# Optimization experiments

Measured on AMD Instinct MI355X. Metric: run time of the kernel, lower is better.

## Reference

```python
import jax, jax.numpy as jnp
import numpy as np

jax.config.update("jax_enable_x64", True)  # original upcasts to double for cdist

B, D, T = 16, 256, 2048
K = 1024  # num_embeddings
COMMITMENT_COST = 0.25


def setup_inputs() -> dict:
    key = jax.random.key(0)
    k1, k2 = jax.random.split(key)
    inputs = jax.random.normal(k1, (B, D, T), dtype=jnp.float32)
    embeddings = jax.random.uniform(k2, (K, D), minval=-1.0 / K, maxval=1.0 / K, dtype=jnp.float32)
    return {"inputs": inputs, "embeddings": embeddings}


def reference(inputs, embeddings):
    b, d, t = inputs.shape
    # [B, D, T] -> [B*T, D]
    flat = jnp.transpose(inputs, (0, 2, 1)).reshape(-1, d)
    # fp64 pairwise squared distances (argmin identical to cdist p=2)
    x = flat.astype(jnp.float64)
    e = embeddings.astype(jnp.float64)
    d2 = (jnp.sum(x * x, axis=1, keepdims=True)
          - 2.0 * (x @ e.T)
          + jnp.sum(e * e, axis=1))  # [N, K]
    encoding_indices = jnp.argmin(d2, axis=1)  # [N]
    quantized = embeddings[encoding_indices].reshape(b, t, d).transpose(0, 2, 1)  # [B, D, T]
    q_detached = jax.lax.stop_gradient(quantized)
    e_latent_loss = jnp.mean((q_detached - inputs) ** 2)
    q_latent_loss = jnp.mean((quantized - jax.lax.stop_gradient(inputs)) ** 2)
    loss = q_latent_loss + COMMITMENT_COST * e_latent_loss
    # straight-through estimator
    quantized_st = inputs + jax.lax.stop_gradient(quantized - inputs)
    return quantized_st, loss, e_latent_loss, q_latent_loss, encoding_indices
```

## Files before the change

kernel.cpp:

```cpp
#include <hip/hip_runtime.h>
#include <hip/hip_bf16.h>

#define NB 16
#define ND 256
#define NT 2048
#define NK 1024
#define NN (NB * NT)
#define QSIZE (NB * ND * NT)
#define SCL_OFF QSIZE
#define IDX_OFF (QSIZE + 3)
#define TAU 4.0e-5f

#define WS_CNT   8
#define WS_E2F   1024
#define WS_E2D   8192
#define WS_IDX   16384
#define WS_LIST  147456
#define WS_BPACK 278528
#define WS_PART  1327104

typedef __attribute__((ext_vector_type(8))) short bf16x8;
typedef __attribute__((ext_vector_type(4))) float f32x4;
#define MFMA16(a, b, c) __builtin_amdgcn_mfma_f32_16x16x32_bf16(a, b, c, 0, 0, 0)

__device__ inline void bf16split(float v, short& hi, short& lo) {
    union { __hip_bfloat16 b; short s; } uh, ul;
    uh.b = __float2bfloat16(v);
    float hf = __bfloat162float(uh.b);
    ul.b = __float2bfloat16(v - hf);
    hi = uh.s; lo = ul.s;
}

__global__ __launch_bounds__(64) void vq_e2(const float4* __restrict__ E4,
                                            double* __restrict__ e2d,
                                            float* __restrict__ e2f,
                                            int* __restrict__ cnt) {
    int k = blockIdx.x;
    int lane = threadIdx.x;
    float4 v = E4[k * 64 + lane];
    double s = (double)v.x * v.x + (double)v.y * v.y + (double)v.z * v.z + (double)v.w * v.w;
    #pragma unroll
    for (int off = 32; off; off >>= 1) s += __shfl_down(s, off, 64);
    if (lane == 0) { e2d[k] = s; e2f[k] = (float)s; }
    if (k == 0 && lane == 0) cnt[0] = 0;
}

__global__ __launch_bounds__(64) void vq_prep_bpack(const float4* __restrict__ E4,
                                                    uint4* __restrict__ Bp4) {
    const int cc = blockIdx.x >> 3;
    const int ds = blockIdx.x & 7;
    const int lane = threadIdx.x;
    const int c = cc * 16 + (lane & 15);
    const int q = lane >> 4;
    float4 v0 = E4[(size_t)c * 64 + ds * 8 + q * 2];
    float4 v1 = E4[(size_t)c * 64 + ds * 8 + q * 2 + 1];
    float vals[8] = {v0.x, v0.y, v0.z, v0.w, v1.x, v1.y, v1.z, v1.w};
    union { short s[8]; uint4 v; } hi, lo;
    #pragma unroll
    for (int j = 0; j < 8; ++j) bf16split(vals[j], hi.s[j], lo.s[j]);
    Bp4[(size_t)cc * 1024 + ds * 64 + lane]       = hi.v;
    Bp4[(size_t)cc * 1024 + 512 + ds * 64 + lane] = lo.v;
}

__global__ __launch_bounds__(256, 1) void vq_pass1(const float* __restrict__ X,
                                                   const uint4* __restrict__ Bp4,
                                                   const float* __restrict__ e2f,
                                                   int* __restrict__ idx_ws,
                                                   int* __restrict__ cnt,
                                                   int* __restrict__ list,
                                                   float* __restrict__ out) {
    __shared__ uint4 Bl4[2][1024];
    const int tid  = threadIdx.x;
    const int lane = tid & 63;
    const int w    = tid >> 6;
    const int n0   = blockIdx.x * 128;
    const int b    = n0 >> 11;
    const int t0   = n0 & (NT - 1);
    const int m16  = lane & 15;
    const int q    = lane >> 4;

    bf16x8 ah[2][8], al[2][8];
    const float* Xb = X + (size_t)b * (ND * NT);
    #pragma unroll
    for (int t = 0; t < 2; ++t) {
        const int trow = t0 + w * 32 + t * 16 + m16;
        #pragma unroll
        for (int ds = 0; ds < 8; ++ds) {
            #pragma unroll
            for (int j = 0; j < 8; ++j) {
                const int d = ds * 32 + q * 8 + j;
                float v = Xb[(size_t)d * NT + trow];
                short h, l; bf16split(v, h, l);
                ah[t][ds][j] = h; al[t][ds][j] = l;
            }
        }
    }

    float b1[2][4], b2[2][4]; int i1[2][4];
    #pragma unroll
    for (int t = 0; t < 2; ++t)
        #pragma unroll
        for (int r = 0; r < 4; ++r) { b1[t][r] = 3e38f; b2[t][r] = 3e38f; i1[t][r] = 0; }

    uint4 pre[4];
    #pragma unroll
    for (int i = 0; i < 4; ++i) pre[i] = Bp4[tid + 256 * i];
    #pragma unroll
    for (int i = 0; i < 4; ++i) Bl4[0][tid + 256 * i] = pre[i];
    __syncthreads();

    for (int cc = 0; cc < 64; ++cc) {
        const bf16x8* Bf = (const bf16x8*)Bl4[cc & 1];
        if (cc < 63) {
            #pragma unroll
            for (int i = 0; i < 4; ++i) pre[i] = Bp4[(size_t)(cc + 1) * 1024 + tid + 256 * i];
        }
        f32x4 hh0 = {0.f,0.f,0.f,0.f}, lh0 = {0.f,0.f,0.f,0.f}, hl0 = {0.f,0.f,0.f,0.f};
        f32x4 hh1 = {0.f,0.f,0.f,0.f}, lh1 = {0.f,0.f,0.f,0.f}, hl1 = {0.f,0.f,0.f,0.f};
        #pragma unroll
        for (int ds = 0; ds < 8; ++ds) {
            bf16x8 bh = Bf[ds * 64 + lane];
            bf16x8 bl = Bf[512 + ds * 64 + lane];
            hh0 = MFMA16(ah[0][ds], bh, hh0);
            hh1 = MFMA16(ah[1][ds], bh, hh1);
            lh0 = MFMA16(al[0][ds], bh, lh0);
            lh1 = MFMA16(al[1][ds], bh, lh1);
            hl0 = MFMA16(ah[0][ds], bl, hl0);
            hl1 = MFMA16(ah[1][ds], bl, hl1);
        }
        if (cc < 63) {
            #pragma unroll
            for (int i = 0; i < 4; ++i) Bl4[(cc + 1) & 1][tid + 256 * i] = pre[i];
            __syncthreads();
        }
        const float e2v = e2f[cc * 16 + m16];
        const int  code = cc * 16 + m16;
        #pragma unroll
        for (int r = 0; r < 4; ++r) {
            float s0 = e2v - 2.0f * (hh0[r] + lh0[r] + hl0[r]);
            if (s0 < b1[0][r]) { b2[0][r] = b1[0][r]; b1[0][r] = s0; i1[0][r] = code; }
            else if (s0 < b2[0][r]) b2[0][r] = s0;
            float s1 = e2v - 2.0f * (hh1[r] + lh1[r] + hl1[r]);
            if (s1 < b1[1][r]) { b2[1][r] = b1[1][r]; b1[1][r] = s1; i1[1][r] = code; }
            else if (s1 < b2[1][r]) b2[1][r] = s1;
        }
    }

    #pragma unroll
    for (int t = 0; t < 2; ++t) {
        #pragma unroll
        for (int r = 0; r < 4; ++r) {
            float B1 = b1[t][r], B2 = b2[t][r]; int I1 = i1[t][r];
            #pragma unroll
            for (int mm = 1; mm < 16; mm <<= 1) {
                float o1 = __shfl_xor(B1, mm, 16);
                float o2 = __shfl_xor(B2, mm, 16);
                int   oi = __shfl_xor(I1, mm, 16);
                if (o1 < B1 || (o1 == B1 && oi < I1)) { B2 = fminf(B1, o2); B1 = o1; I1 = oi; }
                else B2 = fminf(B2, o1);
            }
            if (m16 == 0) {
                int n = n0 + w * 32 + t * 16 + q * 4 + r;
                idx_ws[n] = I1;
                out[IDX_OFF + n] = (float)I1;
                if (B2 - B1 < TAU) { int p = atomicAdd(cnt, 1); list[p] = n; }
            }
        }
    }
}

__global__ __launch_bounds__(256, 2) void vq_refine(const float* __restrict__ X,
                                                    const float4* __restrict__ E4,
                                                    const double* __restrict__ e2d,
                                                    const int* __restrict__ cnt,
                                                    const int* __restrict__ list,
                                                    int* __restrict__ idx_ws,
                                                    float* __restrict__ out) {
    __shared__ double xs[4][256];
    __shared__ double sm_s[4][4];
    __shared__ int    sm_k[4][4];
    const int m = cnt[0];
    const int tid = threadIdx.x;
    for (int p = blockIdx.x; p * 4 < m; p += 512) {
        int nrow[4];
        #pragma unroll
        for (int g = 0; g < 4; ++g) {
            int j = p * 4 + g;
            nrow[g] = list[j < m ? j : m - 1];
        }
        #pragma unroll
        for (int g = 0; g < 4; ++g) {
            int n = nrow[g]; int bb = n >> 11; int tt = n & (NT - 1);
            xs[g][tid] = (double)X[((size_t)bb * ND + tid) * NT + tt];
        }
        __syncthreads();
        double acc[4][4];
        #pragma unroll
        for (int kk = 0; kk < 4; ++kk)
            #pragma unroll
            for (int g = 0; g < 4; ++g) acc[kk][g] = 0.0;
        for (int dq = 0; dq < 64; ++dq) {
            double xv[4][4];
            #pragma unroll
            for (int g = 0; g < 4; ++g)
                #pragma unroll
                for (int c = 0; c < 4; ++c) xv[g][c] = xs[g][dq * 4 + c];
            #pragma unroll
            for (int kk = 0; kk < 4; ++kk) {
                float4 ev = E4[(size_t)(kk * 256 + tid) * 64 + dq];
                double e0 = ev.x, e1 = ev.y, e2 = ev.z, e3 = ev.w;
                #pragma unroll
                for (int g = 0; g < 4; ++g)
                    acc[kk][g] += xv[g][0] * e0 + xv[g][1] * e1 + xv[g][2] * e2 + xv[g][3] * e3;
            }
        }
        #pragma unroll
        for (int g = 0; g < 4; ++g) {
            double bs = 1e300; int bk = 0x7fffffff;
            #pragma unroll
            for (int kk = 0; kk < 4; ++kk) {
                int k = kk * 256 + tid;
                double s = e2d[k] - 2.0 * acc[kk][g];
                if (s < bs) { bs = s; bk = k; }
            }
            #pragma unroll
            for (int mm = 1; mm < 64; mm <<= 1) {
                double os = __shfl_xor(bs, mm, 64);
                int    ok = __shfl_xor(bk, mm, 64);
                if (os < bs || (os == bs && ok < bk)) { bs = os; bk = ok; }
            }
            if ((tid & 63) == 0) { sm_s[tid >> 6][g] = bs; sm_k[tid >> 6][g] = bk; }
        }
        __syncthreads();
        if (tid < 4) {
            double Bv = 1e300; int Kv = 0x7fffffff;
            for (int ww = 0; ww < 4; ++ww) {
                double s2 = sm_s[ww][tid]; int k2 = sm_k[ww][tid];
                if (s2 < Bv || (s2 == Bv && k2 < Kv)) { Bv = s2; Kv = k2; }
            }
            if (p * 4 + tid < m) {
                int n = nrow[tid];
                idx_ws[n] = Kv;
                out[IDX_OFF + n] = (float)Kv;
            }
        }
        __syncthreads();
    }
}

__global__ __launch_bounds__(256) void vq_gather(const float* __restrict__ X,
                                                 const float4* __restrict__ E4,
                                                 const int* __restrict__ idx_ws,
                                                 float* __restrict__ out,
                                                 double* __restrict__ part) {
    __shared__ float Eq[32 * 257];
    __shared__ double sm[4];
    const int bt = blockIdx.x;
    const int b  = bt >> 6;
    const int t0 = (bt & 63) << 5;
    const int* irow = idx_ws + b * NT + t0;
    {
        const int r  = threadIdx.x >> 3;
        const int l8 = threadIdx.x & 7;
        const int id = irow[r];
        const float4* er = E4 + (size_t)id * 64;
        #pragma unroll
        for (int it = 0; it < 8; ++it) {
            int c = l8 + (it << 3);
            float4 v = er[c];
            float* p = &Eq[r * 257 + 4 * c];
            p[0] = v.x; p[1] = v.y; p[2] = v.z; p[3] = v.w;
        }
    }
    __syncthreads();
    const int tw = threadIdx.x & 31;
    const int dg = threadIdx.x >> 5;
    double ls = 0.0;
    #pragma unroll 8
    for (int it = 0; it < 32; ++it) {
        const int d = dg + (it << 3);
        const float qv = Eq[tw * 257 + d];
        const size_t off = ((size_t)b * ND + d) * NT + t0 + tw;
        const float x = X[off];
        out[off] = x + (qv - x);
        const double df = (double)qv - (double)x;
        ls = fma(df, df, ls);
    }
    #pragma unroll
    for (int o = 32; o; o >>= 1) ls += __shfl_down(ls, o, 64);
    if ((threadIdx.x & 63) == 0) sm[threadIdx.x >> 6] = ls;
    __syncthreads();
    if (threadIdx.x == 0) part[bt] = sm[0] + sm[1] + sm[2] + sm[3];
}

__global__ __launch_bounds__(256) void vq_final(const double* __restrict__ part,
                                                float* __restrict__ out) {
    __shared__ double sm[4];
    const int tid = threadIdx.x;
    double s = part[tid] + part[tid + 256] + part[tid + 512] + part[tid + 768];
    #pragma unroll
    for (int o = 32; o; o >>= 1) s += __shfl_down(s, o, 64);
    if ((tid & 63) == 0) sm[tid >> 6] = s;
    __syncthreads();
    if (tid == 0) {
        double mse = (sm[0] + sm[1] + sm[2] + sm[3]) * (1.0 / (double)QSIZE);
        out[SCL_OFF + 0] = (float)(1.25 * mse);
        out[SCL_OFF + 1] = (float)mse;
        out[SCL_OFF + 2] = (float)mse;
    }
}

extern "C" void kernel_launch(void* const* d_in, const int* in_sizes, int n_in,
                              void* d_out, int out_size, void* d_ws, size_t ws_size,
                              hipStream_t stream) {
    const float* X = (const float*)d_in[0];
    const float* E = (const float*)d_in[1];
    float* out = (float*)d_out;

    char* ws = (char*)d_ws;
    int*    cnt   = (int*)   (ws + WS_CNT);
    float*  e2f   = (float*) (ws + WS_E2F);
    double* e2d   = (double*)(ws + WS_E2D);
    int*    idxws = (int*)   (ws + WS_IDX);
    int*    list  = (int*)   (ws + WS_LIST);
    uint4*  bpack = (uint4*) (ws + WS_BPACK);
    double* part  = (double*)(ws + WS_PART);

    vq_e2        <<<NK, 64, 0, stream>>>((const float4*)E, e2d, e2f, cnt);
    vq_prep_bpack<<<512, 64, 0, stream>>>((const float4*)E, bpack);
    vq_pass1     <<<NN / 128, 256, 0, stream>>>(X, bpack, e2f, idxws, cnt, list, out);
    vq_refine    <<<512, 256, 0, stream>>>(X, (const float4*)E, e2d, cnt, list, idxws, out);
    vq_gather    <<<NB * (NT / 32), 256, 0, stream>>>(X, (const float4*)E, idxws, out, part);
    vq_final     <<<1, 256, 0, stream>>>(part, out);
}
```

Baseline: 235.8 us.

## Halve pass1 rows per block and transpose codebook for coalesced refine loads

The first-pass MFMA kernel now handles 64 rows per block instead of 128, halving its per-thread register tile and raising launch bounds to two blocks per CU. The grid doubles, so each block reloads the full packed codebook, doubling codebook traffic into shared memory. Separately, the e2 kernel writes a transposed fp32 codebook so the fp64 refine kernel reads contiguous per-thread codes along d, replacing the strided float4 loads. The transpose adds scattered writes in a small prep kernel.

```diff
diff --git a/kernel.cpp b/kernel.cpp
--- a/kernel.cpp
+++ b/kernel.cpp
@@ -17,7 +17,8 @@
 #define WS_IDX   16384
 #define WS_LIST  147456
 #define WS_BPACK 278528
-#define WS_PART  1327104
+#define WS_ET    1327104
+#define WS_PART  2375680
 
 typedef __attribute__((ext_vector_type(8))) short bf16x8;
 typedef __attribute__((ext_vector_type(4))) float f32x4;
@@ -34,10 +35,15 @@
 __global__ __launch_bounds__(64) void vq_e2(const float4* __restrict__ E4,
                                             double* __restrict__ e2d,
                                             float* __restrict__ e2f,
+                                            float* __restrict__ ET,
                                             int* __restrict__ cnt) {
     int k = blockIdx.x;
     int lane = threadIdx.x;
     float4 v = E4[k * 64 + lane];
+    ET[(size_t)(4 * lane + 0) * NK + k] = v.x;
+    ET[(size_t)(4 * lane + 1) * NK + k] = v.y;
+    ET[(size_t)(4 * lane + 2) * NK + k] = v.z;
+    ET[(size_t)(4 * lane + 3) * NK + k] = v.w;
     double s = (double)v.x * v.x + (double)v.y * v.y + (double)v.z * v.z + (double)v.w * v.w;
     #pragma unroll
     for (int off = 32; off; off >>= 1) s += __shfl_down(s, off, 64);
@@ -62,7 +68,7 @@
     Bp4[(size_t)cc * 1024 + 512 + ds * 64 + lane] = lo.v;
 }
 
-__global__ __launch_bounds__(256, 1) void vq_pass1(const float* __restrict__ X,
+__global__ __launch_bounds__(256, 2) void vq_pass1(const float* __restrict__ X,
                                                    const uint4* __restrict__ Bp4,
                                                    const float* __restrict__ e2f,
                                                    int* __restrict__ idx_ws,
@@ -73,17 +79,16 @@
     const int tid  = threadIdx.x;
     const int lane = tid & 63;
     const int w    = tid >> 6;
-    const int n0   = blockIdx.x * 128;
+    const int n0   = blockIdx.x * 64;
     const int b    = n0 >> 11;
     const int t0   = n0 & (NT - 1);
     const int m16  = lane & 15;
     const int q    = lane >> 4;
 
-    bf16x8 ah[2][8], al[2][8];
+    bf16x8 ah[8], al[8];
     const float* Xb = X + (size_t)b * (ND * NT);
-    #pragma unroll
-    for (int t = 0; t < 2; ++t) {
-        const int trow = t0 + w * 32 + t * 16 + m16;
+    {
+        const int trow = t0 + w * 16 + m16;
         #pragma unroll
         for (int ds = 0; ds < 8; ++ds) {
             #pragma unroll
@@ -91,16 +96,14 @@
                 const int d = ds * 32 + q * 8 + j;
                 float v = Xb[(size_t)d * NT + trow];
                 short h, l; bf16split(v, h, l);
-                ah[t][ds][j] = h; al[t][ds][j] = l;
-            }
-        }
-    }
-
-    float b1[2][4], b2[2][4]; int i1[2][4];
-    #pragma unroll
-    for (int t = 0; t < 2; ++t)
-        #pragma unroll
-        for (int r = 0; r < 4; ++r) { b1[t][r] = 3e38f; b2[t][r] = 3e38f; i1[t][r] = 0; }
+                ah[ds][j] = h; al[ds][j] = l;
+            }
+        }
+    }
+
+    float b1[4], b2[4]; int i1[4];
+    #pragma unroll
+    for (int r = 0; r < 4; ++r) { b1[r] = 3e38f; b2[r] = 3e38f; i1[r] = 0; }
 
     uint4 pre[4];
     #pragma unroll
@@ -115,18 +118,14 @@
             #pragma unroll
             for (int i = 0; i < 4; ++i) pre[i] = Bp4[(size_t)(cc + 1) * 1024 + tid + 256 * i];
         }
-        f32x4 hh0 = {0.f,0.f,0.f,0.f}, lh0 = {0.f,0.f,0.f,0.f}, hl0 = {0.f,0.f,0.f,0.f};
-        f32x4 hh1 = {0.f,0.f,0.f,0.f}, lh1 = {0.f,0.f,0.f,0.f}, hl1 = {0.f,0.f,0.f,0.f};
+        f32x4 hh = {0.f,0.f,0.f,0.f}, lh = {0.f,0.f,0.f,0.f}, hl = {0.f,0.f,0.f,0.f};
         #pragma unroll
         for (int ds = 0; ds < 8; ++ds) {
             bf16x8 bh = Bf[ds * 64 + lane];
             bf16x8 bl = Bf[512 + ds * 64 + lane];
-            hh0 = MFMA16(ah[0][ds], bh, hh0);
-            hh1 = MFMA16(ah[1][ds], bh, hh1);
-            lh0 = MFMA16(al[0][ds], bh, lh0);
-            lh1 = MFMA16(al[1][ds], bh, lh1);
-            hl0 = MFMA16(ah[0][ds], bl, hl0);
-            hl1 = MFMA16(ah[1][ds], bl, hl1);
+            hh = MFMA16(ah[ds], bh, hh);
+            lh = MFMA16(al[ds], bh, lh);
+            hl = MFMA16(ah[ds], bl, hl);
         }
         if (cc < 63) {
             #pragma unroll
@@ -137,40 +136,34 @@
         const int  code = cc * 16 + m16;
         #pragma unroll
         for (int r = 0; r < 4; ++r) {
-            float s0 = e2v - 2.0f * (hh0[r] + lh0[r] + hl0[r]);
-            if (s0 < b1[0][r]) { b2[0][r] = b1[0][r]; b1[0][r] = s0; i1[0][r] = code; }
-            else if (s0 < b2[0][r]) b2[0][r] = s0;
-            float s1 = e2v - 2.0f * (hh1[r] + lh1[r] + hl1[r]);
-            if (s1 < b1[1][r]) { b2[1][r] = b1[1][r]; b1[1][r] = s1; i1[1][r] = code; }
-            else if (s1 < b2[1][r]) b2[1][r] = s1;
-        }
-    }
-
-    #pragma unroll
-    for (int t = 0; t < 2; ++t) {
-        #pragma unroll
-        for (int r = 0; r < 4; ++r) {
-            float B1 = b1[t][r], B2 = b2[t][r]; int I1 = i1[t][r];
-            #pragma unroll
-            for (int mm = 1; mm < 16; mm <<= 1) {
-                float o1 = __shfl_xor(B1, mm, 16);
-                float o2 = __shfl_xor(B2, mm, 16);
-                int   oi = __shfl_xor(I1, mm, 16);
-                if (o1 < B1 || (o1 == B1 && oi < I1)) { B2 = fminf(B1, o2); B1 = o1; I1 = oi; }
-                else B2 = fminf(B2, o1);
-            }
-            if (m16 == 0) {
-                int n = n0 + w * 32 + t * 16 + q * 4 + r;
-                idx_ws[n] = I1;
-                out[IDX_OFF + n] = (float)I1;
-                if (B2 - B1 < TAU) { int p = atomicAdd(cnt, 1); list[p] = n; }
-            }
+            float s0 = e2v - 2.0f * (hh[r] + lh[r] + hl[r]);
+            if (s0 < b1[r]) { b2[r] = b1[r]; b1[r] = s0; i1[r] = code; }
+            else if (s0 < b2[r]) b2[r] = s0;
+        }
+    }
+
+    #pragma unroll
+    for (int r = 0; r < 4; ++r) {
+        float B1 = b1[r], B2 = b2[r]; int I1 = i1[r];
+        #pragma unroll
+        for (int mm = 1; mm < 16; mm <<= 1) {
+            float o1 = __shfl_xor(B1, mm, 16);
+            float o2 = __shfl_xor(B2, mm, 16);
+            int   oi = __shfl_xor(I1, mm, 16);
+            if (o1 < B1 || (o1 == B1 && oi < I1)) { B2 = fminf(B1, o2); B1 = o1; I1 = oi; }
+            else B2 = fminf(B2, o1);
+        }
+        if (m16 == 0) {
+            int n = n0 + w * 16 + q * 4 + r;
+            idx_ws[n] = I1;
+            out[IDX_OFF + n] = (float)I1;
+            if (B2 - B1 < TAU) { int p = atomicAdd(cnt, 1); list[p] = n; }
         }
     }
 }
 
 __global__ __launch_bounds__(256, 2) void vq_refine(const float* __restrict__ X,
-                                                    const float4* __restrict__ E4,
+                                                    const float* __restrict__ ET,
                                                     const double* __restrict__ e2d,
                                                     const int* __restrict__ cnt,
                                                     const int* __restrict__ list,
@@ -199,19 +192,19 @@
         for (int kk = 0; kk < 4; ++kk)
             #pragma unroll
             for (int g = 0; g < 4; ++g) acc[kk][g] = 0.0;
-        for (int dq = 0; dq < 64; ++dq) {
-            double xv[4][4];
-            #pragma unroll
-            for (int g = 0; g < 4; ++g)
-                #pragma unroll
-                for (int c = 0; c < 4; ++c) xv[g][c] = xs[g][dq * 4 + c];
-            #pragma unroll
-            for (int kk = 0; kk < 4; ++kk) {
-                float4 ev = E4[(size_t)(kk * 256 + tid) * 64 + dq];
-                double e0 = ev.x, e1 = ev.y, e2 = ev.z, e3 = ev.w;
-                #pragma unroll
-                for (int g = 0; g < 4; ++g)
-                    acc[kk][g] += xv[g][0] * e0 + xv[g][1] * e1 + xv[g][2] * e2 + xv[g][3] * e3;
+        #pragma unroll 2
+        for (int dd = 0; dd < 256; ++dd) {
+            float e0 = ET[(size_t)dd * NK +   0 + tid];
+            float e1 = ET[(size_t)dd * NK + 256 + tid];
+            float e2 = ET[(size_t)dd * NK + 512 + tid];
+            float e3 = ET[(size_t)dd * NK + 768 + tid];
+            #pragma unroll
+            for (int g = 0; g < 4; ++g) {
+                double xv = xs[g][dd];
+                acc[0][g] += xv * (double)e0;
+                acc[1][g] += xv * (double)e1;
+                acc[2][g] += xv * (double)e2;
+                acc[3][g] += xv * (double)e3;
             }
         }
         #pragma unroll
@@ -324,12 +317,13 @@
     int*    idxws = (int*)   (ws + WS_IDX);
     int*    list  = (int*)   (ws + WS_LIST);
     uint4*  bpack = (uint4*) (ws + WS_BPACK);
+    float*  et    = (float*) (ws + WS_ET);
     double* part  = (double*)(ws + WS_PART);
 
-    vq_e2        <<<NK, 64, 0, stream>>>((const float4*)E, e2d, e2f, cnt);
+    vq_e2        <<<NK, 64, 0, stream>>>((const float4*)E, e2d, e2f, et, cnt);
     vq_prep_bpack<<<512, 64, 0, stream>>>((const float4*)E, bpack);
-    vq_pass1     <<<NN / 128, 256, 0, stream>>>(X, bpack, e2f, idxws, cnt, list, out);
-    vq_refine    <<<512, 256, 0, stream>>>(X, (const float4*)E, e2d, cnt, list, idxws, out);
+    vq_pass1     <<<NN / 64, 256, 0, stream>>>(X, bpack, e2f, idxws, cnt, list, out);
+    vq_refine    <<<512, 256, 0, stream>>>(X, et, e2d, cnt, list, idxws, out);
     vq_gather    <<<NB * (NT / 32), 256, 0, stream>>>(X, (const float4*)E, idxws, out, part);
     vq_final     <<<1, 256, 0, stream>>>(part, out);
 }
```

Result: slower. 263.3 us (+11.7%).

## Split codebook across two pass1 blocks, add merge kernel, transpose E for refine

Applied to the files above, without the earlier changes.

Pass1 now launches twice as many blocks, each scanning half of the codebook, and writes per-slice best, second-best and index to workspace. A new merge kernel combines the two slices, writes indices and builds the refine list. Refine can read a transposed fp32 codebook written by vq_e2 for coalesced loads, used when the workspace is large enough, and gather reads indices from the float output. The aim is better occupancy and more parallelism in pass1, at the cost of reloading and re-splitting X per slice and running an extra kernel.

```diff
diff --git a/kernel.cpp b/kernel.cpp
--- a/kernel.cpp
+++ b/kernel.cpp
@@ -11,13 +11,17 @@
 #define IDX_OFF (QSIZE + 3)
 #define TAU 4.0e-5f
 
-#define WS_CNT   8
-#define WS_E2F   1024
-#define WS_E2D   8192
-#define WS_IDX   16384
-#define WS_LIST  147456
-#define WS_BPACK 278528
-#define WS_PART  1327104
+#define WS_CNT   0
+#define WS_PART  64
+#define WS_E2F   8448
+#define WS_E2D   12544
+#define WS_LIST  20736
+#define WS_B1S   151808
+#define WS_B2S   413952
+#define WS_I1S   676096
+#define WS_BPACK 938240
+#define WS_ET    1986816
+#define WS_NEED_ET (WS_ET + 1048576)
 
 typedef __attribute__((ext_vector_type(8))) short bf16x8;
 typedef __attribute__((ext_vector_type(4))) float f32x4;
@@ -34,10 +38,17 @@
 __global__ __launch_bounds__(64) void vq_e2(const float4* __restrict__ E4,
                                             double* __restrict__ e2d,
                                             float* __restrict__ e2f,
+                                            float* __restrict__ ET, int use_et,
                                             int* __restrict__ cnt) {
     int k = blockIdx.x;
     int lane = threadIdx.x;
     float4 v = E4[k * 64 + lane];
+    if (use_et) {
+        ET[(size_t)(4 * lane + 0) * NK + k] = v.x;
+        ET[(size_t)(4 * lane + 1) * NK + k] = v.y;
+        ET[(size_t)(4 * lane + 2) * NK + k] = v.z;
+        ET[(size_t)(4 * lane + 3) * NK + k] = v.w;
+    }
     double s = (double)v.x * v.x + (double)v.y * v.y + (double)v.z * v.z + (double)v.w * v.w;
     #pragma unroll
     for (int off = 32; off; off >>= 1) s += __shfl_down(s, off, 64);
@@ -62,22 +73,23 @@
     Bp4[(size_t)cc * 1024 + 512 + ds * 64 + lane] = lo.v;
 }
 
-__global__ __launch_bounds__(256, 1) void vq_pass1(const float* __restrict__ X,
+__global__ __launch_bounds__(256, 2) void vq_pass1(const float* __restrict__ X,
                                                    const uint4* __restrict__ Bp4,
                                                    const float* __restrict__ e2f,
-                                                   int* __restrict__ idx_ws,
-                                                   int* __restrict__ cnt,
-                                                   int* __restrict__ list,
-                                                   float* __restrict__ out) {
+                                                   float* __restrict__ b1s,
+                                                   float* __restrict__ b2s,
+                                                   int* __restrict__ i1s) {
     __shared__ uint4 Bl4[2][1024];
-    const int tid  = threadIdx.x;
-    const int lane = tid & 63;
-    const int w    = tid >> 6;
-    const int n0   = blockIdx.x * 128;
-    const int b    = n0 >> 11;
-    const int t0   = n0 & (NT - 1);
-    const int m16  = lane & 15;
-    const int q    = lane >> 4;
+    const int tid   = threadIdx.x;
+    const int lane  = tid & 63;
+    const int w     = tid >> 6;
+    const int slice = blockIdx.x & 1;
+    const int n0    = (blockIdx.x >> 1) * 128;
+    const int b     = n0 >> 11;
+    const int t0    = n0 & (NT - 1);
+    const int m16   = lane & 15;
+    const int q     = lane >> 4;
+    const uint4* Bps = Bp4 + (size_t)slice * 32768;
 
     bf16x8 ah[2][8], al[2][8];
     const float* Xb = X + (size_t)b * (ND * NT);
@@ -104,16 +116,16 @@
 
     uint4 pre[4];
     #pragma unroll
-    for (int i = 0; i < 4; ++i) pre[i] = Bp4[tid + 256 * i];
+    for (int i = 0; i < 4; ++i) pre[i] = Bps[tid + 256 * i];
     #pragma unroll
     for (int i = 0; i < 4; ++i) Bl4[0][tid + 256 * i] = pre[i];
     __syncthreads();
 
-    for (int cc = 0; cc < 64; ++cc) {
+    for (int cc = 0; cc < 32; ++cc) {
         const bf16x8* Bf = (const bf16x8*)Bl4[cc & 1];
-        if (cc < 63) {
-            #pragma unroll
-            for (int i = 0; i < 4; ++i) pre[i] = Bp4[(size_t)(cc + 1) * 1024 + tid + 256 * i];
+        if (cc < 31) {
+            #pragma unroll
+            for (int i = 0; i < 4; ++i) pre[i] = Bps[(size_t)(cc + 1) * 1024 + tid + 256 * i];
         }
         f32x4 hh0 = {0.f,0.f,0.f,0.f}, lh0 = {0.f,0.f,0.f,0.f}, hl0 = {0.f,0.f,0.f,0.f};
         f32x4 hh1 = {0.f,0.f,0.f,0.f}, lh1 = {0.f,0.f,0.f,0.f}, hl1 = {0.f,0.f,0.f,0.f};
@@ -128,13 +140,13 @@
             hl0 = MFMA16(ah[0][ds], bl, hl0);
             hl1 = MFMA16(ah[1][ds], bl, hl1);
         }
-        if (cc < 63) {
+        if (cc < 31) {
             #pragma unroll
             for (int i = 0; i < 4; ++i) Bl4[(cc + 1) & 1][tid + 256 * i] = pre[i];
             __syncthreads();
         }
-        const float e2v = e2f[cc * 16 + m16];
-        const int  code = cc * 16 + m16;
+        const int  code = slice * 512 + cc * 16 + m16;
+        const float e2v = e2f[code];
         #pragma unroll
         for (int r = 0; r < 4; ++r) {
             float s0 = e2v - 2.0f * (hh0[r] + lh0[r] + hl0[r]);
@@ -161,20 +173,35 @@
             }
             if (m16 == 0) {
                 int n = n0 + w * 32 + t * 16 + q * 4 + r;
-                idx_ws[n] = I1;
-                out[IDX_OFF + n] = (float)I1;
-                if (B2 - B1 < TAU) { int p = atomicAdd(cnt, 1); list[p] = n; }
-            }
-        }
-    }
+                int s = slice * NN + n;
+                b1s[s] = B1; b2s[s] = B2; i1s[s] = I1;
+            }
+        }
+    }
+}
+
+__global__ __launch_bounds__(256) void vq_merge(const float* __restrict__ b1s,
+                                                const float* __restrict__ b2s,
+                                                const int* __restrict__ i1s,
+                                                int* __restrict__ cnt,
+                                                int* __restrict__ list,
+                                                float* __restrict__ out) {
+    const int n = blockIdx.x * 256 + threadIdx.x;
+    float a1 = b1s[n],      a2 = b2s[n];      int ai = i1s[n];
+    float c1 = b1s[NN + n], c2 = b2s[NN + n]; int ci = i1s[NN + n];
+    float B1, B2; int I1;
+    if (c1 < a1) { B1 = c1; I1 = ci; B2 = fminf(a1, c2); }
+    else         { B1 = a1; I1 = ai; B2 = fminf(a2, c1); }
+    out[IDX_OFF + n] = (float)I1;
+    if (B2 - B1 < TAU) { int p = atomicAdd(cnt, 1); list[p] = n; }
 }
 
 __global__ __launch_bounds__(256, 2) void vq_refine(const float* __restrict__ X,
                                                     const float4* __restrict__ E4,
+                                                    const float* __restrict__ ET, int use_et,
                                                     const double* __restrict__ e2d,
                                                     const int* __restrict__ cnt,
                                                     const int* __restrict__ list,
-                                                    int* __restrict__ idx_ws,
                                                     float* __restrict__ out) {
     __shared__ double xs[4][256];
     __shared__ double sm_s[4][4];
@@ -199,19 +226,32 @@
         for (int kk = 0; kk < 4; ++kk)
             #pragma unroll
             for (int g = 0; g < 4; ++g) acc[kk][g] = 0.0;
-        for (int dq = 0; dq < 64; ++dq) {
-            double xv[4][4];
-            #pragma unroll
-            for (int g = 0; g < 4; ++g)
+        if (use_et) {
+            #pragma unroll 2
+            for (int dd = 0; dd < 256; ++dd) {
+                float e0 = ET[(size_t)dd * NK +   0 + tid];
+                float e1 = ET[(size_t)dd * NK + 256 + tid];
+                float e2 = ET[(size_t)dd * NK + 512 + tid];
+                float e3 = ET[(size_t)dd * NK + 768 + tid];
                 #pragma unroll
-                for (int c = 0; c < 4; ++c) xv[g][c] = xs[g][dq * 4 + c];
-            #pragma unroll
-            for (int kk = 0; kk < 4; ++kk) {
-                float4 ev = E4[(size_t)(kk * 256 + tid) * 64 + dq];
-                double e0 = ev.x, e1 = ev.y, e2 = ev.z, e3 = ev.w;
+                for (int g = 0; g < 4; ++g) {
+                    double xv = xs[g][dd];
+                    acc[0][g] += xv * (double)e0;
+                    acc[1][g] += xv * (double)e1;
+                    acc[2][g] += xv * (double)e2;
+                    acc[3][g] += xv * (double)e3;
+                }
+            }
+        } else {
+            for (int dq = 0; dq < 64; ++dq) {
                 #pragma unroll
-                for (int g = 0; g < 4; ++g)
-                    acc[kk][g] += xv[g][0] * e0 + xv[g][1] * e1 + xv[g][2] * e2 + xv[g][3] * e3;
+                for (int kk = 0; kk < 4; ++kk) {
+                    float4 ev = E4[(size_t)(kk * 256 + tid) * 64 + dq];
+                    #pragma unroll
+                    for (int g = 0; g < 4; ++g)
+                        acc[kk][g] += xs[g][dq*4+0] * (double)ev.x + xs[g][dq*4+1] * (double)ev.y
+                                    + xs[g][dq*4+2] * (double)ev.z + xs[g][dq*4+3] * (double)ev.w;
+                }
             }
         }
         #pragma unroll
@@ -238,11 +278,7 @@
                 double s2 = sm_s[ww][tid]; int k2 = sm_k[ww][tid];
                 if (s2 < Bv || (s2 == Bv && k2 < Kv)) { Bv = s2; Kv = k2; }
             }
-            if (p * 4 + tid < m) {
-                int n = nrow[tid];
-                idx_ws[n] = Kv;
-                out[IDX_OFF + n] = (float)Kv;
-            }
+            if (p * 4 + tid < m) out[IDX_OFF + nrow[tid]] = (float)Kv;
         }
         __syncthreads();
     }
@@ -250,7 +286,6 @@
 
 __global__ __launch_bounds__(256) void vq_gather(const float* __restrict__ X,
                                                  const float4* __restrict__ E4,
-                                                 const int* __restrict__ idx_ws,
                                                  float* __restrict__ out,
                                                  double* __restrict__ part) {
     __shared__ float Eq[32 * 257];
@@ -258,11 +293,11 @@
     const int bt = blockIdx.x;
     const int b  = bt >> 6;
     const int t0 = (bt & 63) << 5;
-    const int* irow = idx_ws + b * NT + t0;
+    const float* irowf = out + IDX_OFF + b * NT + t0;
     {
         const int r  = threadIdx.x >> 3;
         const int l8 = threadIdx.x & 7;
-        const int id = irow[r];
+        const int id = (int)irowf[r];
         const float4* er = E4 + (size_t)id * 64;
         #pragma unroll
         for (int it = 0; it < 8; ++it) {
@@ -319,17 +354,22 @@
 
     char* ws = (char*)d_ws;
     int*    cnt   = (int*)   (ws + WS_CNT);
+    double* part  = (double*)(ws + WS_PART);
     float*  e2f   = (float*) (ws + WS_E2F);
     double* e2d   = (double*)(ws + WS_E2D);
-    int*    idxws = (int*)   (ws + WS_IDX);
     int*    list  = (int*)   (ws + WS_LIST);
+    float*  b1s   = (float*) (ws + WS_B1S);
+    float*  b2s   = (float*) (ws + WS_B2S);
+    int*    i1s   = (int*)   (ws + WS_I1S);
     uint4*  bpack = (uint4*) (ws + WS_BPACK);
-    double* part  = (double*)(ws + WS_PART);
-
-    vq_e2        <<<NK, 64, 0, stream>>>((const float4*)E, e2d, e2f, cnt);
+    float*  et    = (float*) (ws + WS_ET);
+    const int use_et = (ws_size >= (size_t)WS_NEED_ET) ? 1 : 0;
+
+    vq_e2        <<<NK, 64, 0, stream>>>((const float4*)E, e2d, e2f, et, use_et, cnt);
     vq_prep_bpack<<<512, 64, 0, stream>>>((const float4*)E, bpack);
-    vq_pass1     <<<NN / 128, 256, 0, stream>>>(X, bpack, e2f, idxws, cnt, list, out);
-    vq_refine    <<<512, 256, 0, stream>>>(X, (const float4*)E, e2d, cnt, list, idxws, out);
-    vq_gather    <<<NB * (NT / 32), 256, 0, stream>>>(X, (const float4*)E, idxws, out, part);
+    vq_pass1     <<<NN / 64, 256, 0, stream>>>(X, bpack, e2f, b1s, b2s, i1s);
+    vq_merge     <<<NN / 256, 256, 0, stream>>>(b1s, b2s, i1s, cnt, list, out);
+    vq_refine    <<<512, 256, 0, stream>>>(X, (const float4*)E, et, use_et, e2d, cnt, list, out);
+    vq_gather    <<<NB * (NT / 32), 256, 0, stream>>>(X, (const float4*)E, out, part);
     vq_final     <<<1, 256, 0, stream>>>(part, out);
 }
```

Measured after the change: 216.2 us. 8.3% less time.
